# Kernel optimization log

Hardware: AMD Instinct MI355X
Metric: run time of the kernel (lower is better)

## Reference

```python
import jax, jax.numpy as jnp
import numpy as np

K = 32
EPS = 1e-5  # BatchNorm eps; eval mode with running_mean=0, running_var=1


def knn_idx(x):
    # x: [B, C, N] -> idx of K nearest neighbors [B, N, K]
    inner = -2.0 * jnp.einsum('bcn,bcm->bnm', x, x)
    xx = jnp.sum(x * x, axis=1)  # [B, N]
    pd = -xx[:, :, None] - inner - xx[:, None, :]  # negative squared dist
    return jax.lax.top_k(pd, K)[1]


def get_neighbors(x):
    # x: [B, C, N] -> edge features [B, N, K, 2C] (nbr - ctr, ctr)
    idx = knn_idx(x)
    xt = jnp.transpose(x, (0, 2, 1))  # [B, N, C]
    nbrs = jax.vmap(lambda p, i: p[i])(xt, idx)  # [B, N, K, C]
    ctr = jnp.broadcast_to(xt[:, :, None, :], nbrs.shape)
    return jnp.concatenate([nbrs - ctr, ctr], axis=-1)


def bn_eval(h, g, b, nd):
    # inference-mode BN, running_mean=0, running_var=1
    shape = [1, -1] + [1] * (nd - 2)
    return h * (g / jnp.sqrt(1.0 + EPS)).reshape(shape) + b.reshape(shape)


def edge_conv(x, W, g, b):
    # x: [B, C, N] -> [B, O, N]; 1x1 conv over edge feats + BN + LeakyReLU + max over K
    feat = get_neighbors(x)  # [B, N, K, 2C]
    h = jnp.einsum('bnkc,oc->bonk', feat, W)
    h = jax.nn.leaky_relu(bn_eval(h, g, b, 4), 0.2)
    return jnp.max(h, axis=-1)


def setup_inputs():
    key = jax.random.key(0)
    ks = jax.random.split(key, 40)
    B, N = 4, 2048

    def rn(i, shape, s=0.1):
        return jax.random.normal(ks[i], shape, jnp.float32) * s

    def gm(i, c):
        return 1.0 + rn(i, (c,))

    inp = {
        'x': jax.random.normal(ks[0], (B, 3, N), jnp.float32),
        'l': jax.random.normal(ks[1], (B, 5), jnp.float32),
        'n': jax.random.normal(ks[2], (B, 7), jnp.float32),
        'W1': rn(3, (64, 6)), 'g1': gm(4, 64), 'b1': rn(5, (64,)),
        'W2': rn(6, (64, 128)), 'g2': gm(7, 64), 'b2': rn(8, (64,)),
        'W3': rn(9, (128, 128)), 'g3': gm(10, 128), 'b3': rn(11, (128,)),
        'W4': rn(12, (256, 256)), 'g4': gm(13, 256), 'b4': rn(14, (256,)),
        'W5': rn(15, (1024, 512)), 'g5': gm(16, 1024), 'b5': rn(17, (1024,)),
        'W6': rn(18, (64, 5)), 'g6': gm(19, 64), 'b6': rn(20, (64,)),
        'W7': rn(21, (64, 7)), 'g7': gm(22, 64), 'b7': rn(23, (64,)),
        'L1': rn(24, (512, 1152)), 'g8': gm(25, 512), 'b8': rn(26, (512,)),
        'L2': rn(27, (256, 512)), 'L2b': rn(28, (256,)), 'g9': gm(29, 256), 'b9': rn(30, (256,)),
        'L3': rn(31, (28, 256)), 'L3b': rn(32, (28,)),
    }
    return inp


def reference(x, l, n, W1, g1, b1, W2, g2, b2, W3, g3, b3, W4, g4, b4,
              W5, g5, b5, W6, g6, b6, W7, g7, b7,
              L1, g8, b8, L2, L2b, g9, b9, L3, L3b):
    x1 = edge_conv(x, W1, g1, b1)    # [B, 64, N]
    x2 = edge_conv(x1, W2, g2, b2)   # [B, 64, N]
    x3 = edge_conv(x2, W3, g3, b3)   # [B, 128, N]
    x4 = edge_conv(x3, W4, g4, b4)   # [B, 256, N]
    cat = jnp.concatenate([x1, x2, x3, x4], axis=1)  # [B, 512, N]
    h = jnp.einsum('bcn,oc->bon', cat, W5)
    h = jax.nn.leaky_relu(bn_eval(h, g5, b5, 3), 0.2)
    h = jnp.max(h, axis=-1)  # global max pool -> [B, 1024]
    lf = jax.nn.leaky_relu(bn_eval(jnp.einsum('bc,oc->bo', l, W6), g6, b6, 2), 0.2)
    nf = jax.nn.leaky_relu(bn_eval(jnp.einsum('bc,oc->bo', n, W7), g7, b7, 2), 0.2)
    v = jnp.concatenate([h, lf, nf], axis=-1)  # [B, 1152]
    v = jax.nn.relu(bn_eval(v @ L1.T, g8, b8, 2))  # dropout = identity (eval)
    v = jax.nn.relu(bn_eval(v @ L2.T + L2b, g9, b9, 2))
    return v @ L3.T + L3b  # [B, 28]
```

## Files before the change

kernel.cpp:

```cpp
#include <hip/hip_runtime.h>
#include <hip/hip_bf16.h>

#define NPTS 2048
#define NB 4
#define KNN 32
#define NIN 33

static __device__ __forceinline__ float b2f(__hip_bfloat16 v) { return __bfloat162float(v); }
#define ISQ 0.99999499996875f

typedef __attribute__((ext_vector_type(8))) short short8v;
typedef __attribute__((ext_vector_type(4))) float f32x4;

static __device__ __forceinline__ unsigned ordkey(float f) {
  unsigned u = __float_as_uint(f);
  return u ^ (unsigned)(((int)u >> 31) | 0x80000000);
}

static __device__ __forceinline__ void loadv(const float* p, float (&d)[1]) { d[0] = *p; }
static __device__ __forceinline__ void loadv(const float* p, float (&d)[2]) {
  float2 v = *(const float2*)p; d[0] = v.x; d[1] = v.y;
}
static __device__ __forceinline__ void loadv(const float* p, float (&d)[4]) {
  float4 v = *(const float4*)p; d[0] = v.x; d[1] = v.y; d[2] = v.z; d[3] = v.w;
}

static __device__ __forceinline__ float wave_red_sum(float s) {
#pragma unroll
  for (int off = 32; off > 0; off >>= 1) s += __shfl_xor(s, off);
  return s;
}

__global__ __launch_bounds__(64) void detect_kernel(const unsigned short* __restrict__ x,
                                                    int* __restrict__ flag) {
  int cnt = 0;
  for (int i = threadIdx.x; i < 512; i += 64) {
    unsigned e = (x[i] >> 7) & 0xFFu;
    if (e >= 0xC6u) cnt++;
  }
#pragma unroll
  for (int off = 32; off > 0; off >>= 1) cnt += __shfl_down(cnt, off);
  if (threadIdx.x == 0) flag[0] = (cnt == 0) ? 1 : 0;
}

struct CvtArgs {
  const void* src[NIN];
  int off[NIN + 1];
};

__global__ __launch_bounds__(256) void cvt_all_kernel(CvtArgs a, float* __restrict__ out,
                                                      int total, int nb1,
                                                      __hip_bfloat16* __restrict__ w5bf,
                                                      const int* __restrict__ flag) {
  if ((int)blockIdx.x < nb1) {
    int t = blockIdx.x * 256 + threadIdx.x;
    if (t >= total) return;
    int s = 0;
    while (t >= a.off[s + 1]) s++;
    int j = t - a.off[s];
    float v;
    if (flag[0]) v = b2f(((const __hip_bfloat16*)a.src[s])[j]);
    else         v = ((const float*)a.src[s])[j];
    out[t] = v;
  } else {
    int t = (blockIdx.x - nb1) * 256 + threadIdx.x;
    if (flag[0]) w5bf[t] = ((const __hip_bfloat16*)a.src[15])[t];
    else         w5bf[t] = __float2bfloat16(((const float*)a.src[15])[t]);
  }
}

template <int C>
__global__ __launch_bounds__(256) void xx_kernel(const float* __restrict__ x, long bstride,
                                                 float* __restrict__ xx) {
  int t = blockIdx.x * 256 + threadIdx.x;
  int b = t / NPTS, m = t % NPTS;
  const float* xb = x + (long)b * bstride + m;
  float s = 0.f;
#pragma unroll
  for (int c = 0; c < C; ++c) { float v = xb[(long)c * NPTS]; s = fmaf(v, v, s); }
  xx[t] = s;
}

template <int C>
__global__ __launch_bounds__(256) void pdgemmsym_kernel(const float* __restrict__ x, long bstride,
                                                        const float* __restrict__ xx,
                                                        unsigned* __restrict__ keys) {
  constexpr int KT = (C < 16) ? C : 16;
  __shared__ __align__(16) float At[KT][64];
  __shared__ __align__(16) float Bt[KT][64];
  __shared__ __align__(16) unsigned Ts[64][68];
  int t = blockIdx.x;
  int tj = (int)((sqrtf(8.f * (float)t + 1.f) - 1.f) * 0.5f);
  while ((tj + 1) * (tj + 2) / 2 <= t) tj++;
  while (tj * (tj + 1) / 2 > t) tj--;
  int ti = t - tj * (tj + 1) / 2;
  int n0 = ti * 64, m0 = tj * 64;
  int tid = threadIdx.x, tx = tid & 15, ty = tid >> 4;
  const float* xb = x + (long)blockIdx.y * bstride;
  float acc[4][4] = {};
  for (int k0 = 0; k0 < C; k0 += KT) {
    for (int lin = tid; lin < KT * 64; lin += 256) {
      int r = lin >> 6, col = lin & 63;
      At[r][col] = xb[(long)(k0 + r) * NPTS + n0 + col];
      Bt[r][col] = xb[(long)(k0 + r) * NPTS + m0 + col];
    }
    __syncthreads();
#pragma unroll
    for (int kc = 0; kc < KT; ++kc) {
      float4 av = *(const float4*)&At[kc][ty * 4];
      float4 bv = *(const float4*)&Bt[kc][tx * 4];
      acc[0][0] = fmaf(av.x, bv.x, acc[0][0]); acc[0][1] = fmaf(av.x, bv.y, acc[0][1]);
      acc[0][2] = fmaf(av.x, bv.z, acc[0][2]); acc[0][3] = fmaf(av.x, bv.w, acc[0][3]);
      acc[1][0] = fmaf(av.y, bv.x, acc[1][0]); acc[1][1] = fmaf(av.y, bv.y, acc[1][1]);
      acc[1][2] = fmaf(av.y, bv.z, acc[1][2]); acc[1][3] = fmaf(av.y, bv.w, acc[1][3]);
      acc[2][0] = fmaf(av.z, bv.x, acc[2][0]); acc[2][1] = fmaf(av.z, bv.y, acc[2][1]);
      acc[2][2] = fmaf(av.z, bv.z, acc[2][2]); acc[2][3] = fmaf(av.z, bv.w, acc[2][3]);
      acc[3][0] = fmaf(av.w, bv.x, acc[3][0]); acc[3][1] = fmaf(av.w, bv.y, acc[3][1]);
      acc[3][2] = fmaf(av.w, bv.z, acc[3][2]); acc[3][3] = fmaf(av.w, bv.w, acc[3][3]);
    }
    __syncthreads();
  }
  const float* xxq = xx + (long)blockIdx.y * NPTS;
  float4 xxm = *(const float4*)&xxq[m0 + tx * 4];
  unsigned* kb = keys + ((long)blockIdx.y << 22);
  unsigned ok[4][4];
#pragma unroll
  for (int i = 0; i < 4; ++i) {
    float xxn = xxq[n0 + ty * 4 + i];
    ok[i][0] = ordkey((-xxn - (-2.f * acc[i][0])) - xxm.x);
    ok[i][1] = ordkey((-xxn - (-2.f * acc[i][1])) - xxm.y);
    ok[i][2] = ordkey((-xxn - (-2.f * acc[i][2])) - xxm.z);
    ok[i][3] = ordkey((-xxn - (-2.f * acc[i][3])) - xxm.w);
    uint4 o = make_uint4(ok[i][0], ok[i][1], ok[i][2], ok[i][3]);
    *(uint4*)&kb[(long)(n0 + ty * 4 + i) * NPTS + m0 + tx * 4] = o;
  }
  if (ti != tj) {
#pragma unroll
    for (int i = 0; i < 4; ++i)
#pragma unroll
      for (int j = 0; j < 4; ++j) Ts[tx * 4 + j][ty * 4 + i] = ok[i][j];
    __syncthreads();
#pragma unroll
    for (int i = 0; i < 4; ++i)
      *(uint4*)&kb[(long)(m0 + ty * 4 + i) * NPTS + n0 + tx * 4] =
          *(const uint4*)&Ts[ty * 4 + i][tx * 4];
  }
}

__global__ __launch_bounds__(256) void select_kernel(const unsigned* __restrict__ keys,
                                                     int* __restrict__ idxout) {
  int wave = threadIdx.x >> 6, lane = threadIdx.x & 63;
  int q = blockIdx.x * 4 + wave;
  int bloc = q >> 11, n = q & 2047;
  const uint4* rp = (const uint4*)(keys + ((long)((bloc << 11) | n) << 11));
  unsigned K[32];
#pragma unroll
  for (int t = 0; t < 8; ++t) {
    uint4 kk = rp[t * 64 + lane];
    K[4 * t + 0] = kk.x; K[4 * t + 1] = kk.y; K[4 * t + 2] = kk.z; K[4 * t + 3] = kk.w;
  }
  unsigned t0 = 0, t1 = 0, t2 = 0, t3 = 0;
#pragma unroll
  for (int s = 0; s < 32; ++s) {
    unsigned k = K[s];
    if (k > t3) {
      if (k > t1) {
        if (k > t0) { t3 = t2; t2 = t1; t1 = t0; t0 = k; }
        else        { t3 = t2; t2 = t1; t1 = k; }
      } else {
        if (k > t2) { t3 = t2; t2 = k; }
        else        { t3 = k; }
      }
    }
  }
  unsigned orv = t0 | t1 | t2 | t3, andv = t0 & t1 & t2 & t3;
#pragma unroll
  for (int xm = 32; xm >= 1; xm >>= 1) {
    orv  |= __shfl_xor(orv, xm);
    andv &= __shfl_xor(andv, xm);
  }
  unsigned V = orv ^ andv;
  unsigned P = andv & ~V;
  int need = KNN;
  for (int b = 31; b >= 0; --b) {
    unsigned bit = 1u << b;
    if (!(V & bit)) continue;
    unsigned hm = 0xFFFFFFFFu << b;
    unsigned Pb = (P & hm) | bit;
    int c = (int)__popcll(__ballot((t0 & hm) == Pb)) +
            (int)__popcll(__ballot((t1 & hm) == Pb)) +
            (int)__popcll(__ballot((t2 & hm) == Pb)) +
            (int)__popcll(__ballot((t3 & hm) == Pb));
    if (c >= need) P |= bit;
    else need -= c;
  }
  int cg = 0;
#pragma unroll
  for (int s = 0; s < 32; ++s) cg += (int)__popcll(__ballot(K[s] > P));
  if (cg > KNN - 1) {
    unsigned orf = K[0], anf = K[0];
#pragma unroll
    for (int s = 1; s < 32; ++s) { orf |= K[s]; anf &= K[s]; }
#pragma unroll
    for (int xm = 32; xm >= 1; xm >>= 1) {
      orf |= __shfl_xor(orf, xm);
      anf &= __shfl_xor(anf, xm);
    }
    unsigned Vf = orf ^ anf;
    P = anf & ~Vf;
    need = KNN;
    for (int b = 31; b >= 0; --b) {
      unsigned bit = 1u << b;
      if (!(Vf & bit)) continue;
      unsigned hm = 0xFFFFFFFFu << b;
      unsigned Pb = (P & hm) | bit;
      int c = 0;
#pragma unroll
      for (int s = 0; s < 32; ++s) c += (int)__popcll(__ballot((K[s] & hm) == Pb));
      if (c >= need) P |= bit;
      else need -= c;
    }
  }
  int* orow = idxout + ((bloc << 11) | n) * KNN;
  int base = 0;
  unsigned eqmask = 0;
#pragma unroll
  for (int s = 0; s < 32; ++s) {
    bool take = K[s] > P;
    unsigned long long bal = __ballot(take);
    if (take) {
      int pos = base + (int)__popcll(bal & ((1ull << lane) - 1ull));
      orow[pos] = ((s >> 2) << 8) + lane * 4 + (s & 3);
    }
    base += (int)__popcll(bal);
    if (K[s] == P) eqmask |= (1u << s);
  }
  int rem = KNN - base;
  for (int it = 0; it < rem; ++it) {
    unsigned mym = 0xFFFFFFFFu;
    if (eqmask) {
      int s = __ffs(eqmask) - 1;
      mym = (unsigned)(((s >> 2) << 8) + lane * 4 + (s & 3));
    }
    unsigned wm = mym;
#pragma unroll
    for (int xm = 32; xm >= 1; xm >>= 1) {
      unsigned o = __shfl_xor(wm, xm);
      wm = o < wm ? o : wm;
    }
    if (mym == wm) {
      orow[base + it] = (int)wm;
      eqmask &= eqmask - 1;
    }
  }
}

template <int C>
__global__ __launch_bounds__(256) void yzt_kernel(const float* __restrict__ x, long bstride,
                                                  const float* __restrict__ W, int O,
                                                  float* __restrict__ yt, float* __restrict__ zt) {
  constexpr int KT = (C < 16) ? C : 16;
  __shared__ __align__(16) float Xs[KT][64];
  __shared__ __align__(16) float Wy[KT][64];
  __shared__ __align__(16) float Wp[KT][64];
  int b = blockIdx.z, m0 = blockIdx.y * 64, o0 = blockIdx.x * 64;
  int tid = threadIdx.x, tx = tid & 15, ty = tid >> 4;
  const float* xb = x + (long)b * bstride;
  const int twoC = 2 * C;
  float accy[4][4] = {}, accp[4][4] = {};
  for (int k0 = 0; k0 < C; k0 += KT) {
    for (int lin = tid; lin < KT * 64; lin += 256) {
      int r = lin >> 6, col = lin & 63;
      Xs[r][col] = xb[(long)(k0 + r) * NPTS + m0 + col];
      float wy = W[(o0 + col) * twoC + k0 + r];
      Wy[r][col] = wy;
      Wp[r][col] = W[(o0 + col) * twoC + C + k0 + r] - wy;
    }
    __syncthreads();
#pragma unroll
    for (int kc = 0; kc < KT; ++kc) {
      float4 wv = *(const float4*)&Wy[kc][tx * 4];
      float4 pv = *(const float4*)&Wp[kc][tx * 4];
      float xm[4];
      xm[0] = Xs[kc][ty * 4 + 0]; xm[1] = Xs[kc][ty * 4 + 1];
      xm[2] = Xs[kc][ty * 4 + 2]; xm[3] = Xs[kc][ty * 4 + 3];
#pragma unroll
      for (int i = 0; i < 4; ++i) {
        accy[i][0] = fmaf(xm[i], wv.x, accy[i][0]);
        accy[i][1] = fmaf(xm[i], wv.y, accy[i][1]);
        accy[i][2] = fmaf(xm[i], wv.z, accy[i][2]);
        accy[i][3] = fmaf(xm[i], wv.w, accy[i][3]);
        accp[i][0] = fmaf(xm[i], pv.x, accp[i][0]);
        accp[i][1] = fmaf(xm[i], pv.y, accp[i][1]);
        accp[i][2] = fmaf(xm[i], pv.z, accp[i][2]);
        accp[i][3] = fmaf(xm[i], pv.w, accp[i][3]);
      }
    }
    __syncthreads();
  }
#pragma unroll
  for (int i = 0; i < 4; ++i) {
    long base = ((long)b * NPTS + m0 + ty * 4 + i) * O + o0 + tx * 4;
    *(float4*)&yt[base] = make_float4(accy[i][0], accy[i][1], accy[i][2], accy[i][3]);
    *(float4*)&zt[base] = make_float4(accp[i][0], accp[i][1], accp[i][2], accp[i][3]);
  }
}

template <int RO>
__global__ __launch_bounds__(256) void gmaxt_kernel(const float* __restrict__ yt,
                                                    const float* __restrict__ zt,
                                                    const int* __restrict__ idx,
                                                    const float* __restrict__ g,
                                                    const float* __restrict__ bb,
                                                    float* __restrict__ out, long obstride,
                                                    float* __restrict__ xxout,
                                                    __hip_bfloat16* __restrict__ catbf, int loff) {
  constexpr int O = RO * 64;
  int wave = threadIdx.x >> 6, lane = threadIdx.x & 63;
  int n = blockIdx.x * 4 + wave, b = blockIdx.y;
  int jreg = idx[((b << 11) + n) * KNN + (lane & 31)];
  int obase = lane * RO;
  float gs[RO], bs[RO], zr[RO], acc[RO];
  loadv(zt + ((long)(b << 11) + n) * O + obase, zr);
#pragma unroll
  for (int r = 0; r < RO; ++r) {
    gs[r] = g[obase + r] * ISQ;
    bs[r] = bb[obase + r];
    acc[r] = -INFINITY;
  }
  const float* yb = yt + ((long)(b << 11)) * O + obase;
#pragma unroll
  for (int k = 0; k < KNN; ++k) {
    int j = __shfl(jreg, k);
    float yv[RO];
    loadv(yb + (long)j * O, yv);
#pragma unroll
    for (int r = 0; r < RO; ++r) {
      float v = fmaf(gs[r], yv[r] + zr[r], bs[r]);
      v = v >= 0.f ? v : 0.2f * v;
      acc[r] = fmaxf(acc[r], v);
    }
  }
  float* op = out + (long)b * obstride + (long)obase * NPTS + n;
#pragma unroll
  for (int r = 0; r < RO; ++r) op[(long)r * NPTS] = acc[r];
  __hip_bfloat16* cb = catbf + ((long)(b << 11) + n) * 512 + loff + obase;
#pragma unroll
  for (int r = 0; r < RO; ++r) cb[r] = __float2bfloat16(acc[r]);
  if (xxout) {
    float ss = 0.f;
#pragma unroll
    for (int r = 0; r < RO; ++r) ss = fmaf(acc[r], acc[r], ss);
    ss = wave_red_sum(ss);
    if (lane == 0) xxout[(b << 11) + n] = ss;
  }
}

__global__ __launch_bounds__(256) void gemm5m_kernel(const __hip_bfloat16* __restrict__ catbf,
                                                     const __hip_bfloat16* __restrict__ w5bf,
                                                     const float* __restrict__ g5,
                                                     const float* __restrict__ b5,
                                                     float* __restrict__ pmax) {
  __shared__ __align__(16) short Bs[2][8 * 64 * 8];
  int b = blockIdx.z, po0 = blockIdx.y * 128, n0 = blockIdx.x * 64;
  int wave = threadIdx.x >> 6, lane = threadIdx.x & 63;
  int quad = lane >> 4, l15 = lane & 15;
  const short* cbase = (const short*)catbf + ((long)(b << 11) + n0) * 512;
  const short* abase0 = (const short*)w5bf + (long)(po0 + wave * 32 + l15) * 512 + quad * 8;
  const short* abase1 = abase0 + 16 * 512;
  const short* bsrc0 = cbase + (long)lane * 512 + (2 * wave + 0) * 8;
  const short* bsrc1 = cbase + (long)lane * 512 + (2 * wave + 1) * 8;
  short* bdst0 = &Bs[0][((2 * wave + 0) * 64 + lane) * 8];
  short* bdst1 = &Bs[0][((2 * wave + 1) * 64 + lane) * 8];
  const int bufstride = 8 * 64 * 8;

  short8v Br[2][2], Ar[2][2][2];
  f32x4 acc[2][4] = {};

  Br[0][0] = *(const short8v*)(bsrc0);
  Br[0][1] = *(const short8v*)(bsrc1);
#pragma unroll
  for (int h = 0; h < 2; ++h)
#pragma unroll
    for (int j = 0; j < 2; ++j)
      Ar[0][h][j] = *(const short8v*)((h ? abase1 : abase0) + j * 32);
  *(short8v*)bdst0 = Br[0][0];
  *(short8v*)bdst1 = Br[0][1];
  Br[1][0] = *(const short8v*)(bsrc0 + 64);
  Br[1][1] = *(const short8v*)(bsrc1 + 64);
#pragma unroll
  for (int h = 0; h < 2; ++h)
#pragma unroll
    for (int j = 0; j < 2; ++j)
      Ar[1][h][j] = *(const short8v*)((h ? abase1 : abase0) + 64 + j * 32);
  __syncthreads();

  for (int it = 0; it < 8; ++it) {
    int cur = it & 1;
    const short* lb = &Bs[cur][0];
#pragma unroll
    for (int j = 0; j < 2; ++j) {
#pragma unroll
      for (int nt = 0; nt < 4; ++nt) {
        short8v bf = *(const short8v*)(lb + ((j * 4 + quad) * 64 + nt * 16 + l15) * 8);
        acc[0][nt] = __builtin_amdgcn_mfma_f32_16x16x32_bf16(Ar[cur][0][j], bf, acc[0][nt], 0, 0, 0);
        acc[1][nt] = __builtin_amdgcn_mfma_f32_16x16x32_bf16(Ar[cur][1][j], bf, acc[1][nt], 0, 0, 0);
      }
    }
    if (it < 7) {
      if (it < 6) {
        int ks = (it + 2) * 64;
        Br[cur][0] = *(const short8v*)(bsrc0 + ks);
        Br[cur][1] = *(const short8v*)(bsrc1 + ks);
#pragma unroll
        for (int h = 0; h < 2; ++h)
#pragma unroll
          for (int j = 0; j < 2; ++j)
            Ar[cur][h][j] = *(const short8v*)((h ? abase1 : abase0) + ks + j * 32);
      }
      int nb = cur ^ 1;
      *(short8v*)(bdst0 + nb * bufstride) = Br[nb][0];
      *(short8v*)(bdst1 + nb * bufstride) = Br[nb][1];
      __syncthreads();
    }
  }

#pragma unroll
  for (int h = 0; h < 2; ++h) {
#pragma unroll
    for (int r = 0; r < 4; ++r) {
      int po = po0 + wave * 32 + h * 16 + quad * 4 + r;
      float sc = g5[po] * ISQ;
      float bi = b5[po];
      float mx = -INFINITY;
#pragma unroll
      for (int nt = 0; nt < 4; ++nt) {
        float v = fmaf(sc, acc[h][nt][r], bi);
        v = v >= 0.f ? v : 0.2f * v;
        mx = fmaxf(mx, v);
      }
#pragma unroll
      for (int xm = 1; xm < 16; xm <<= 1) mx = fmaxf(mx, __shfl_xor(mx, xm));
      if (l15 == 0) pmax[(long)(b * 1024 + po) * 32 + blockIdx.x] = mx;
    }
  }
}

__global__ __launch_bounds__(256) void redlfnf_kernel(const float* __restrict__ pmax,
                                                      const float* __restrict__ l,
                                                      const float* __restrict__ nn,
                                                      const float* __restrict__ W6,
                                                      const float* __restrict__ g6,
                                                      const float* __restrict__ b6,
                                                      const float* __restrict__ W7,
                                                      const float* __restrict__ g7,
                                                      const float* __restrict__ b7,
                                                      float* __restrict__ v) {
  if (blockIdx.x < 16) {
    int t = blockIdx.x * 256 + threadIdx.x;
    float mx = -INFINITY;
#pragma unroll
    for (int j = 0; j < 32; ++j) mx = fmaxf(mx, pmax[(long)t * 32 + j]);
    int b = t >> 10, po = t & 1023;
    v[b * 1152 + po] = mx;
  } else {
    int idx = (blockIdx.x - 16) * 256 + threadIdx.x;
    int b = idx >> 7, t = idx & 127;
    if (t < 64) {
      float s = 0.f;
#pragma unroll
      for (int c = 0; c < 5; ++c) s = fmaf(W6[t * 5 + c], l[b * 5 + c], s);
      float val = fmaf(g6[t] * ISQ, s, b6[t]);
      v[b * 1152 + 1024 + t] = val >= 0.f ? val : 0.2f * val;
    } else {
      int o = t - 64;
      float s = 0.f;
#pragma unroll
      for (int c = 0; c < 7; ++c) s = fmaf(W7[o * 7 + c], nn[b * 7 + c], s);
      float val = fmaf(g7[o] * ISQ, s, b7[o]);
      v[b * 1152 + 1088 + o] = val >= 0.f ? val : 0.2f * val;
    }
  }
}

__global__ __launch_bounds__(256) void head1_kernel(const float* __restrict__ v,
                                                    const float* __restrict__ L1,
                                                    const float* __restrict__ g8,
                                                    const float* __restrict__ b8,
                                                    float* __restrict__ v1) {
  int wave = threadIdx.x >> 6, lane = threadIdx.x & 63;
  int t = blockIdx.x * 4 + wave;
  int b = t >> 9, o = t & 511;
  const float* vb = v + b * 1152;
  const float* wr = L1 + (long)o * 1152;
  float s = 0.f;
#pragma unroll
  for (int c = lane; c < 1152; c += 64) s = fmaf(wr[c], vb[c], s);
  s = wave_red_sum(s);
  if (lane == 0) {
    float val = fmaf(g8[o] * ISQ, s, b8[o]);
    v1[t] = fmaxf(val, 0.f);
  }
}

__global__ __launch_bounds__(256) void head2_kernel(const float* __restrict__ v1,
                                                    const float* __restrict__ L2,
                                                    const float* __restrict__ L2b,
                                                    const float* __restrict__ g9,
                                                    const float* __restrict__ b9,
                                                    float* __restrict__ v2) {
  int wave = threadIdx.x >> 6, lane = threadIdx.x & 63;
  int t = blockIdx.x * 4 + wave;
  int b = t >> 8, o = t & 255;
  const float* vb = v1 + b * 512;
  const float* wr = L2 + (long)o * 512;
  float s = 0.f;
#pragma unroll
  for (int c = lane; c < 512; c += 64) s = fmaf(wr[c], vb[c], s);
  s = wave_red_sum(s);
  if (lane == 0) {
    float sv = s + L2b[o];
    float val = fmaf(g9[o] * ISQ, sv, b9[o]);
    v2[t] = fmaxf(val, 0.f);
  }
}

__global__ __launch_bounds__(256) void head3_kernel(const float* __restrict__ v2,
                                                    const float* __restrict__ L3,
                                                    const float* __restrict__ L3b,
                                                    void* __restrict__ out,
                                                    const int* __restrict__ flag) {
  int wave = threadIdx.x >> 6, lane = threadIdx.x & 63;
  int t = blockIdx.x * 4 + wave;
  if (t >= 112) return;
  int b = t / 28, o = t % 28;
  const float* vb = v2 + b * 256;
  const float* wr = L3 + o * 256;
  float s = 0.f;
#pragma unroll
  for (int c = lane; c < 256; c += 64) s = fmaf(wr[c], vb[c], s);
  s = wave_red_sum(s);
  if (lane == 0) {
    float sv = s + L3b[o];
    if (flag[0]) ((__hip_bfloat16*)out)[t] = __float2bfloat16(sv);
    else         ((float*)out)[t] = sv;
  }
}

extern "C" void kernel_launch(void* const* d_in, const int* in_sizes, int n_in,
                              void* d_out, int out_size, void* d_ws, size_t ws_size,
                              hipStream_t stream) {
  CvtArgs ca;
  int off[NIN + 1];
  off[0] = 0;
  for (int i = 0; i < NIN; ++i) {
    ca.src[i] = d_in[i];
    off[i + 1] = off[i] + in_sizes[i];
    ca.off[i] = off[i];
  }
  ca.off[NIN] = off[NIN];
  const int total = off[NIN];

  int* flag = (int*)d_ws;
  float* fin = (float*)((char*)d_ws + 64);
  const float* xf  = fin + off[0];
  const float* lf  = fin + off[1];
  const float* nf  = fin + off[2];
  const float* W1f = fin + off[3];  const float* g1f = fin + off[4];  const float* b1f = fin + off[5];
  const float* W2f = fin + off[6];  const float* g2f = fin + off[7];  const float* b2f_ = fin + off[8];
  const float* W3f = fin + off[9];  const float* g3f = fin + off[10]; const float* b3f = fin + off[11];
  const float* W4f = fin + off[12]; const float* g4f = fin + off[13]; const float* b4f = fin + off[14];
  const float* g5f = fin + off[16]; const float* b5f = fin + off[17];
  const float* W6f = fin + off[18]; const float* g6f = fin + off[19]; const float* b6f = fin + off[20];
  const float* W7f = fin + off[21]; const float* g7f = fin + off[22]; const float* b7f = fin + off[23];
  const float* L1f = fin + off[24]; const float* g8f = fin + off[25]; const float* b8f = fin + off[26];
  const float* L2f = fin + off[27]; const float* L2bf = fin + off[28];
  const float* g9f = fin + off[29]; const float* b9f = fin + off[30];
  const float* L3f = fin + off[31]; const float* L3bf = fin + off[32];

  float* p = fin + ((total + 15) & ~15);
  float* cat  = p;
  float* yb   = cat + 4 * 512 * NPTS;
  float* zb   = yb + 4 * 256 * NPTS;
  float* xxb  = zb + 4 * 256 * NPTS;
  int*   idxb = (int*)(xxb + 4 * NPTS);
  float* pmax = (float*)(idxb + 4 * NPTS * KNN);
  float* vb   = pmax + 4 * 1024 * 32;
  float* v1b  = vb + 4 * 1152;
  float* v2b  = v1b + 4 * 512;
  __hip_bfloat16* w5bf  = (__hip_bfloat16*)(v2b + 4 * 256);
  __hip_bfloat16* catbf = w5bf + 1024 * 512;
  unsigned* keys_tail = (unsigned*)(catbf + (size_t)4 * NPTS * 512);

  size_t need_full = (size_t)((char*)(keys_tail + (size_t)NB * NPTS * NPTS) - (char*)d_ws);
  int bpass = (ws_size >= need_full) ? NB : 1;
  unsigned* keys = (bpass == NB) ? keys_tail : (unsigned*)yb;

  const long bst1 = 3L * NPTS;
  const long bstc = 512L * NPTS;
  const int NTRI = 32 * 33 / 2;
  const int nb1 = (total + 255) / 256;

  detect_kernel<<<1, 64, 0, stream>>>((const unsigned short*)d_in[0], flag);
  cvt_all_kernel<<<nb1 + 2048, 256, 0, stream>>>(ca, fin, total, nb1, w5bf, flag);

  xx_kernel<3><<<32, 256, 0, stream>>>(xf, bst1, xxb);
  for (int b0 = 0; b0 < NB; b0 += bpass) {
    pdgemmsym_kernel<3><<<dim3(NTRI, bpass), 256, 0, stream>>>(xf + b0 * bst1, bst1, xxb + b0 * NPTS, keys);
    select_kernel<<<512 * bpass, 256, 0, stream>>>(keys, idxb + (long)b0 * NPTS * KNN);
  }
  yzt_kernel<3><<<dim3(1, 32, NB), 256, 0, stream>>>(xf, bst1, W1f, 64, yb, zb);
  gmaxt_kernel<1><<<dim3(512, NB), 256, 0, stream>>>(yb, zb, idxb, g1f, b1f, cat, bstc, xxb, catbf, 0);

  for (int b0 = 0; b0 < NB; b0 += bpass) {
    pdgemmsym_kernel<64><<<dim3(NTRI, bpass), 256, 0, stream>>>(cat + b0 * bstc, bstc, xxb + b0 * NPTS, keys);
    select_kernel<<<512 * bpass, 256, 0, stream>>>(keys, idxb + (long)b0 * NPTS * KNN);
  }
  yzt_kernel<64><<<dim3(1, 32, NB), 256, 0, stream>>>(cat, bstc, W2f, 64, yb, zb);
  gmaxt_kernel<1><<<dim3(512, NB), 256, 0, stream>>>(yb, zb, idxb, g2f, b2f_, cat + 64L * NPTS, bstc, xxb, catbf, 64);

  for (int b0 = 0; b0 < NB; b0 += bpass) {
    pdgemmsym_kernel<64><<<dim3(NTRI, bpass), 256, 0, stream>>>(cat + 64L * NPTS + b0 * bstc, bstc, xxb + b0 * NPTS, keys);
    select_kernel<<<512 * bpass, 256, 0, stream>>>(keys, idxb + (long)b0 * NPTS * KNN);
  }
  yzt_kernel<64><<<dim3(2, 32, NB), 256, 0, stream>>>(cat + 64L * NPTS, bstc, W3f, 128, yb, zb);
  gmaxt_kernel<2><<<dim3(512, NB), 256, 0, stream>>>(yb, zb, idxb, g3f, b3f, cat + 128L * NPTS, bstc, xxb, catbf, 128);

  for (int b0 = 0; b0 < NB; b0 += bpass) {
    pdgemmsym_kernel<128><<<dim3(NTRI, bpass), 256, 0, stream>>>(cat + 128L * NPTS + b0 * bstc, bstc, xxb + b0 * NPTS, keys);
    select_kernel<<<512 * bpass, 256, 0, stream>>>(keys, idxb + (long)b0 * NPTS * KNN);
  }
  yzt_kernel<128><<<dim3(4, 32, NB), 256, 0, stream>>>(cat + 128L * NPTS, bstc, W4f, 256, yb, zb);
  gmaxt_kernel<4><<<dim3(512, NB), 256, 0, stream>>>(yb, zb, idxb, g4f, b4f, cat + 256L * NPTS, bstc, (float*)nullptr, catbf, 256);

  gemm5m_kernel<<<dim3(32, 8, NB), 256, 0, stream>>>(catbf, w5bf, g5f, b5f, pmax);
  redlfnf_kernel<<<18, 256, 0, stream>>>(pmax, lf, nf, W6f, g6f, b6f, W7f, g7f, b7f, vb);

  head1_kernel<<<512, 256, 0, stream>>>(vb, L1f, g8f, b8f, v1b);
  head2_kernel<<<256, 256, 0, stream>>>(v1b, L2f, L2bf, g9f, b9f, v2b);
  head3_kernel<<<28, 256, 0, stream>>>(v2b, L3f, L3bf, d_out, flag);
}
```

Before: 539.3 us.

## Enlarge symmetric pairwise-distance GEMM tile to 128x128 with 8x8 per-thread outputs

The symmetric distance/key kernel now uses 128x128 tiles, with each thread computing an 8x8 register block instead of 4x4. Shared-memory columns are interleaved even/odd so each thread's rows and columns can be read as two float4s. The transposed mirror tile is now written straight from registers rather than staged through shared memory. This cuts the number of blocks and the shared-memory traffic per FMA, at the cost of more registers, fewer blocks for the small-C layers, and less coalesced transposed stores.

```diff
diff --git a/kernel.cpp b/kernel.cpp
--- a/kernel.cpp
+++ b/kernel.cpp
@@ -86,64 +86,82 @@
                                                         const float* __restrict__ xx,
                                                         unsigned* __restrict__ keys) {
   constexpr int KT = (C < 16) ? C : 16;
-  __shared__ __align__(16) float At[KT][64];
-  __shared__ __align__(16) float Bt[KT][64];
-  __shared__ __align__(16) unsigned Ts[64][68];
+  __shared__ __align__(16) float At[KT][128];
+  __shared__ __align__(16) float Bt[KT][128];
   int t = blockIdx.x;
   int tj = (int)((sqrtf(8.f * (float)t + 1.f) - 1.f) * 0.5f);
   while ((tj + 1) * (tj + 2) / 2 <= t) tj++;
   while (tj * (tj + 1) / 2 > t) tj--;
   int ti = t - tj * (tj + 1) / 2;
-  int n0 = ti * 64, m0 = tj * 64;
+  int n0 = ti * 128, m0 = tj * 128;
   int tid = threadIdx.x, tx = tid & 15, ty = tid >> 4;
   const float* xb = x + (long)blockIdx.y * bstride;
-  float acc[4][4] = {};
+  float acc[8][8] = {};
   for (int k0 = 0; k0 < C; k0 += KT) {
-    for (int lin = tid; lin < KT * 64; lin += 256) {
-      int r = lin >> 6, col = lin & 63;
-      At[r][col] = xb[(long)(k0 + r) * NPTS + n0 + col];
-      Bt[r][col] = xb[(long)(k0 + r) * NPTS + m0 + col];
+    for (int lin = tid; lin < KT * 128; lin += 256) {
+      int r = lin >> 7, col = lin & 127;
+      int cm = ((col & 1) << 6) + (col >> 1);
+      At[r][cm] = xb[(long)(k0 + r) * NPTS + n0 + col];
+      Bt[r][cm] = xb[(long)(k0 + r) * NPTS + m0 + col];
     }
     __syncthreads();
 #pragma unroll
     for (int kc = 0; kc < KT; ++kc) {
-      float4 av = *(const float4*)&At[kc][ty * 4];
-      float4 bv = *(const float4*)&Bt[kc][tx * 4];
-      acc[0][0] = fmaf(av.x, bv.x, acc[0][0]); acc[0][1] = fmaf(av.x, bv.y, acc[0][1]);
-      acc[0][2] = fmaf(av.x, bv.z, acc[0][2]); acc[0][3] = fmaf(av.x, bv.w, acc[0][3]);
-      acc[1][0] = fmaf(av.y, bv.x, acc[1][0]); acc[1][1] = fmaf(av.y, bv.y, acc[1][1]);
-      acc[1][2] = fmaf(av.y, bv.z, acc[1][2]); acc[1][3] = fmaf(av.y, bv.w, acc[1][3]);
-      acc[2][0] = fmaf(av.z, bv.x, acc[2][0]); acc[2][1] = fmaf(av.z, bv.y, acc[2][1]);
-      acc[2][2] = fmaf(av.z, bv.z, acc[2][2]); acc[2][3] = fmaf(av.z, bv.w, acc[2][3]);
-      acc[3][0] = fmaf(av.w, bv.x, acc[3][0]); acc[3][1] = fmaf(av.w, bv.y, acc[3][1]);
-      acc[3][2] = fmaf(av.w, bv.z, acc[3][2]); acc[3][3] = fmaf(av.w, bv.w, acc[3][3]);
+      float4 ae = *(const float4*)&At[kc][ty * 4];
+      float4 ao = *(const float4*)&At[kc][64 + ty * 4];
+      float4 be = *(const float4*)&Bt[kc][tx * 4];
+      float4 bo = *(const float4*)&Bt[kc][64 + tx * 4];
+      float av[8] = {ae.x, ae.y, ae.z, ae.w, ao.x, ao.y, ao.z, ao.w};
+      float bv[8] = {be.x, be.y, be.z, be.w, bo.x, bo.y, bo.z, bo.w};
+#pragma unroll
+      for (int ii = 0; ii < 8; ++ii)
+#pragma unroll
+        for (int jj = 0; jj < 8; ++jj)
+          acc[ii][jj] = fmaf(av[ii], bv[jj], acc[ii][jj]);
     }
     __syncthreads();
   }
   const float* xxq = xx + (long)blockIdx.y * NPTS;
-  float4 xxm = *(const float4*)&xxq[m0 + tx * 4];
+  float xxn[8], xxm[8];
+#pragma unroll
+  for (int u = 0; u < 8; ++u) {
+    int pu = (u < 4) ? 2 * u : 2 * (u - 4) + 1;
+    xxn[u] = xxq[n0 + ty * 8 + pu];
+    xxm[u] = xxq[m0 + tx * 8 + pu];
+  }
+#pragma unroll
+  for (int ii = 0; ii < 8; ++ii)
+#pragma unroll
+    for (int jj = 0; jj < 8; ++jj) {
+      float pdv = (-xxn[ii] - (-2.f * acc[ii][jj])) - xxm[jj];
+      acc[ii][jj] = __uint_as_float(ordkey(pdv));
+    }
   unsigned* kb = keys + ((long)blockIdx.y << 22);
-  unsigned ok[4][4];
-#pragma unroll
-  for (int i = 0; i < 4; ++i) {
-    float xxn = xxq[n0 + ty * 4 + i];
-    ok[i][0] = ordkey((-xxn - (-2.f * acc[i][0])) - xxm.x);
-    ok[i][1] = ordkey((-xxn - (-2.f * acc[i][1])) - xxm.y);
-    ok[i][2] = ordkey((-xxn - (-2.f * acc[i][2])) - xxm.z);
-    ok[i][3] = ordkey((-xxn - (-2.f * acc[i][3])) - xxm.w);
-    uint4 o = make_uint4(ok[i][0], ok[i][1], ok[i][2], ok[i][3]);
-    *(uint4*)&kb[(long)(n0 + ty * 4 + i) * NPTS + m0 + tx * 4] = o;
+#pragma unroll
+  for (int ii = 0; ii < 8; ++ii) {
+    int pii = (ii < 4) ? 2 * ii : 2 * (ii - 4) + 1;
+    long rbase = (long)(n0 + ty * 8 + pii) * NPTS + m0 + tx * 8;
+    uint4 w0, w1;
+    w0.x = __float_as_uint(acc[ii][0]); w0.y = __float_as_uint(acc[ii][4]);
+    w0.z = __float_as_uint(acc[ii][1]); w0.w = __float_as_uint(acc[ii][5]);
+    w1.x = __float_as_uint(acc[ii][2]); w1.y = __float_as_uint(acc[ii][6]);
+    w1.z = __float_as_uint(acc[ii][3]); w1.w = __float_as_uint(acc[ii][7]);
+    *(uint4*)&kb[rbase] = w0;
+    *(uint4*)&kb[rbase + 4] = w1;
   }
   if (ti != tj) {
 #pragma unroll
-    for (int i = 0; i < 4; ++i)
-#pragma unroll
-      for (int j = 0; j < 4; ++j) Ts[tx * 4 + j][ty * 4 + i] = ok[i][j];
-    __syncthreads();
-#pragma unroll
-    for (int i = 0; i < 4; ++i)
-      *(uint4*)&kb[(long)(m0 + ty * 4 + i) * NPTS + n0 + tx * 4] =
-          *(const uint4*)&Ts[ty * 4 + i][tx * 4];
+    for (int jj = 0; jj < 8; ++jj) {
+      int pjj = (jj < 4) ? 2 * jj : 2 * (jj - 4) + 1;
+      long rbase = (long)(m0 + tx * 8 + pjj) * NPTS + n0 + ty * 8;
+      uint4 w0, w1;
+      w0.x = __float_as_uint(acc[0][jj]); w0.y = __float_as_uint(acc[4][jj]);
+      w0.z = __float_as_uint(acc[1][jj]); w0.w = __float_as_uint(acc[5][jj]);
+      w1.x = __float_as_uint(acc[2][jj]); w1.y = __float_as_uint(acc[6][jj]);
+      w1.z = __float_as_uint(acc[3][jj]); w1.w = __float_as_uint(acc[7][jj]);
+      *(uint4*)&kb[rbase] = w0;
+      *(uint4*)&kb[rbase + 4] = w1;
+    }
   }
 }
 
@@ -598,7 +616,7 @@
 
   const long bst1 = 3L * NPTS;
   const long bstc = 512L * NPTS;
-  const int NTRI = 32 * 33 / 2;
+  const int NTRI = 16 * 17 / 2;
   const int nb1 = (total + 255) / 256;
 
   detect_kernel<<<1, 64, 0, stream>>>((const unsigned short*)d_in[0], flag);
```

Measured after the change: 583.4 us. 1.08x slower.
